# Optimization experiments

Measured on AMD Instinct MI355X. Metric: run time of the kernel, lower is better.

The kernel has to match this reference:

```python
import jax, jax.numpy as jnp
import numpy as np

S, D, H = 2048, 2048, 16
HD = D // H  # head dim = 128
LN_EPS = 1e-5


def _ln(x, g, b):
    mu = jnp.mean(x, axis=-1, keepdims=True)
    var = jnp.var(x, axis=-1, keepdims=True)
    return (x - mu) / jnp.sqrt(var + LN_EPS) * g + b


def setup_inputs() -> dict:
    key = jax.random.key(0)
    ks = jax.random.split(key, 8)
    B = 2
    s = 0.02  # weight init scale
    return {
        "x": jax.random.normal(ks[0], (B, S, D), jnp.float32),
        "Wq": jax.random.normal(ks[1], (D, D), jnp.float32) * s,
        "bq": jnp.zeros((D,), jnp.float32),
        "Wk": jax.random.normal(ks[2], (D, D), jnp.float32) * s,
        "bk": jnp.zeros((D,), jnp.float32),
        "Wv": jax.random.normal(ks[3], (D, D), jnp.float32) * s,
        "bv": jnp.zeros((D,), jnp.float32),
        "Wo": jax.random.normal(ks[4], (D, D), jnp.float32) * s,
        "bo": jnp.zeros((D,), jnp.float32),
        "ln1_g": jnp.ones((D,), jnp.float32),
        "ln1_b": jnp.zeros((D,), jnp.float32),
        "ln2_g": jnp.ones((D,), jnp.float32),
        "ln2_b": jnp.zeros((D,), jnp.float32),
        "W1": jax.random.normal(ks[5], (4 * D, D), jnp.float32) * s,
        "b1": jnp.zeros((4 * D,), jnp.float32),
        "W2": jax.random.normal(ks[6], (D, 4 * D), jnp.float32) * s,
        "b2": jnp.zeros((D,), jnp.float32),
    }


def reference(x, Wq, bq, Wk, bk, Wv, bv, Wo, bo,
              ln1_g, ln1_b, ln2_g, ln2_b, W1, b1, W2, b2):
    causal = jnp.tril(jnp.ones((S, S), bool))  # [S, S] lower-triangular mask
    neg = jnp.finfo(x.dtype).min
    inv_sqrt_hd = 1.0 / jnp.sqrt(jnp.asarray(HD, x.dtype))

    def block(xs):  # xs: [S, D] (equinox module is per-sequence; vmapped over batch)
        h = _ln(xs, ln1_g, ln1_b)
        q = (h @ Wq.T + bq).reshape(S, H, HD)
        k = (h @ Wk.T + bk).reshape(S, H, HD)
        v = (h @ Wv.T + bv).reshape(S, H, HD)
        logits = jnp.einsum('shd,Shd->hsS', q, k) * inv_sqrt_hd
        logits = jnp.where(causal, logits, neg)
        attn = jax.nn.softmax(logits, axis=-1)
        o = jnp.einsum('hsS,Shd->shd', attn, v).reshape(S, D)
        h = h + (o @ Wo.T + bo)          # residual of post-ln1 value (as in source)
        h2 = _ln(h, ln2_g, ln2_b)
        m = jax.nn.gelu(h2 @ W1.T + b1) @ W2.T + b2
        return h2 + m                    # residual of post-ln2 value (as in source)

    return jax.vmap(block)(x)
```

## Files before the change

### kernel.cpp

```cpp
#include <hip/hip_runtime.h>
#include <hip/hip_bf16.h>
#include <math.h>

#define DD   2048
#define SS   2048
#define HH   16
#define HDIM 128
#define BB   2
#define MM   4096
#define D4   8192

using bf16x8 = __attribute__((ext_vector_type(8))) short;
using f32x4  = __attribute__((ext_vector_type(4))) float;
using f32x16 = __attribute__((ext_vector_type(16))) float;

__device__ __forceinline__ ushort f2bf(float x) {
  uint u = __builtin_bit_cast(uint, x);
  u += 0x7FFFu + ((u >> 16) & 1u);
  return (ushort)(u >> 16);
}
__device__ __forceinline__ float bf2f(ushort u) {
  return __builtin_bit_cast(float, (uint)u << 16);
}
__device__ __forceinline__ uint pkbf2(float a, float b) {
  return (uint)f2bf(a) | ((uint)f2bf(b) << 16);
}

__device__ __forceinline__ float gelu_f(float v) {
  float u = 0.7978845608028654f * (v + 0.044715f * v * v * v);
  float e = __expf(2.0f * u);
  float th = 1.0f - 2.0f / (e + 1.0f);
  return 0.5f * v * (1.0f + th);
}

__device__ __forceinline__ void gload_lds16(const void* g, void* l) {
  __builtin_amdgcn_global_load_lds(
      (const __attribute__((address_space(1))) void*)g,
      (__attribute__((address_space(3))) void*)l, 16, 0, 0);
}

template <int SHIFT>
__global__ __launch_bounds__(256) void cvt4_f32_bf16(
    const float* __restrict__ s0, const float* __restrict__ s1,
    const float* __restrict__ s2, const float* __restrict__ s3,
    ushort* __restrict__ dst) {
  int seg = blockIdx.x >> SHIFT;
  int i = ((blockIdx.x & ((1 << SHIFT) - 1)) << 8) + threadIdx.x;
  const float* src = (seg == 0) ? s0 : (seg == 1) ? s1 : (seg == 2) ? s2 : s3;
  float4 v = ((const float4*)src)[i];
  ushort4 o;
  o.x = f2bf(v.x); o.y = f2bf(v.y); o.z = f2bf(v.z); o.w = f2bf(v.w);
  ((ushort4*)dst)[((size_t)seg << (SHIFT + 8)) + i] = o;
}

template <bool BIN>
__global__ __launch_bounds__(256) void ln_rows(
    const void* __restrict__ inp, const float* __restrict__ gam,
    const float* __restrict__ bet, ushort* __restrict__ outb) {
  int row = blockIdx.x;
  int t = threadIdx.x;
  float v[8];
  if (BIN) {
    const ushort4* r4 = (const ushort4*)((const ushort*)inp + (size_t)row * DD);
    ushort4 a = r4[t * 2], b = r4[t * 2 + 1];
    v[0] = bf2f(a.x); v[1] = bf2f(a.y); v[2] = bf2f(a.z); v[3] = bf2f(a.w);
    v[4] = bf2f(b.x); v[5] = bf2f(b.y); v[6] = bf2f(b.z); v[7] = bf2f(b.w);
  } else {
    const float4* r4 = (const float4*)((const float*)inp + (size_t)row * DD);
    float4 a = r4[t * 2], b = r4[t * 2 + 1];
    v[0] = a.x; v[1] = a.y; v[2] = a.z; v[3] = a.w;
    v[4] = b.x; v[5] = b.y; v[6] = b.z; v[7] = b.w;
  }
  float s = ((v[0] + v[1]) + (v[2] + v[3])) + ((v[4] + v[5]) + (v[6] + v[7]));
  __shared__ float redA[4], redB[4];
  #pragma unroll
  for (int off = 32; off >= 1; off >>= 1) s += __shfl_xor(s, off);
  if ((t & 63) == 0) redA[t >> 6] = s;
  __syncthreads();
  float mean = (redA[0] + redA[1] + redA[2] + redA[3]) * (1.0f / DD);
  float q = 0.f;
  #pragma unroll
  for (int i = 0; i < 8; i++) { v[i] -= mean; q += v[i] * v[i]; }
  #pragma unroll
  for (int off = 32; off >= 1; off >>= 1) q += __shfl_xor(q, off);
  if ((t & 63) == 0) redB[t >> 6] = q;
  __syncthreads();
  float var = (redB[0] + redB[1] + redB[2] + redB[3]) * (1.0f / DD);
  float rstd = rsqrtf(var + 1e-5f);
  const float4* g4 = (const float4*)gam;
  const float4* b4 = (const float4*)bet;
  float4 g0 = g4[t * 2], g1 = g4[t * 2 + 1];
  float4 bb0 = b4[t * 2], bb1 = b4[t * 2 + 1];
  ushort4 u0, u1;
  u0.x = f2bf(v[0] * rstd * g0.x + bb0.x);
  u0.y = f2bf(v[1] * rstd * g0.y + bb0.y);
  u0.z = f2bf(v[2] * rstd * g0.z + bb0.z);
  u0.w = f2bf(v[3] * rstd * g0.w + bb0.w);
  u1.x = f2bf(v[4] * rstd * g1.x + bb1.x);
  u1.y = f2bf(v[5] * rstd * g1.y + bb1.y);
  u1.z = f2bf(v[6] * rstd * g1.z + bb1.z);
  u1.w = f2bf(v[7] * rstd * g1.w + bb1.w);
  ushort4* ob4 = (ushort4*)(outb + (size_t)row * DD);
  ob4[t * 2] = u0; ob4[t * 2 + 1] = u1;
}

template <int OMODE, bool GELU_, bool RES_>
__global__ __launch_bounds__(512, 2) void gemm2(
    const ushort* __restrict__ A, const ushort* __restrict__ Bt,
    const float* __restrict__ pb0, const float* __restrict__ pb1,
    const float* __restrict__ pb2, const ushort* __restrict__ res,
    void* __restrict__ Cout, int M, int N, int K) {
  extern __shared__ __align__(16) ushort smem[];
  const int nbm = M >> 8, nbn = N >> 7;
  const int nwg = nbm * nbn;
  int wg = blockIdx.x;
  int wg2 = (wg & 7) * (nwg >> 3) + (wg >> 3);
  int bm = wg2 % nbm, bn = wg2 / nbm;
  int m0 = bm << 8, n0 = bn << 7;
  int t = threadIdx.x, lane = t & 63, w = t >> 6;
  int wm = w >> 2, wn = w & 3;
  int lr = lane & 15, lg = lane >> 4;

  auto stage = [&](int kt, int slot) {
    int k0 = kt << 6;
    ushort* lA = smem + slot * 24576;
    ushort* lB = lA + 16384;
    #pragma unroll
    for (int r = 0; r < 4; r++) {
      int idx = (r << 9) + t;
      int row = idx >> 3, ch = idx & 7;
      gload_lds16(A + (size_t)(m0 + row) * K + k0 + ((ch ^ (row & 7)) << 3),
                  lA + idx * 8);
    }
    #pragma unroll
    for (int r = 0; r < 2; r++) {
      int idx = (r << 9) + t;
      int row = idx >> 3, ch = idx & 7;
      gload_lds16(Bt + (size_t)(n0 + row) * K + k0 + ((ch ^ (row & 7)) << 3),
                  lB + idx * 8);
    }
  };

  f32x4 acc[8][2] = {};
  const int NT = K >> 6;
  stage(0, 0);
  stage(1, 1);
  int slot = 0;
  for (int kt = 0; kt < NT; ++kt) {
    __builtin_amdgcn_sched_barrier(0);
    if (kt + 1 < NT)
      asm volatile("s_waitcnt vmcnt(6)" ::: "memory");
    else
      asm volatile("s_waitcnt vmcnt(0)" ::: "memory");
    __builtin_amdgcn_s_barrier();
    __builtin_amdgcn_sched_barrier(0);
    if (kt + 2 < NT) {
      int s2 = slot + 2; if (s2 >= 3) s2 -= 3;
      stage(kt + 2, s2);
    }
    const ushort* lA = smem + slot * 24576;
    const ushort* lB = lA + 16384;
    bf16x8 af[8][2], bfr[2][2];
    #pragma unroll
    for (int mi = 0; mi < 8; mi++) {
      int row = wm * 128 + mi * 16 + lr;
      #pragma unroll
      for (int ks = 0; ks < 2; ks++)
        af[mi][ks] = *(const bf16x8*)
            &lA[row * 64 + (((ks * 4 + lg) ^ (row & 7)) << 3)];
    }
    #pragma unroll
    for (int ni = 0; ni < 2; ni++) {
      int row = wn * 32 + ni * 16 + lr;
      #pragma unroll
      for (int ks = 0; ks < 2; ks++)
        bfr[ni][ks] = *(const bf16x8*)
            &lB[row * 64 + (((ks * 4 + lg) ^ (row & 7)) << 3)];
    }
    __builtin_amdgcn_s_setprio(1);
    #pragma unroll
    for (int ks = 0; ks < 2; ks++)
      #pragma unroll
      for (int mi = 0; mi < 8; mi++)
        #pragma unroll
        for (int ni = 0; ni < 2; ni++)
          acc[mi][ni] = __builtin_amdgcn_mfma_f32_16x16x32_bf16(
              af[mi][ks], bfr[ni][ks], acc[mi][ni], 0, 0, 0);
    __builtin_amdgcn_s_setprio(0);
    slot = (slot + 1 == 3) ? 0 : slot + 1;
  }

  if (OMODE == 3) {
    int seg = n0 >> 11;
    const float* pb = (seg == 0) ? pb0 : (seg == 1) ? pb1 : pb2;
    int c0 = n0 & 2047;
    float bv[2];
    #pragma unroll
    for (int ni = 0; ni < 2; ni++) bv[ni] = pb[c0 + wn * 32 + ni * 16 + lr];
    if (seg < 2) {
      ushort* q_or_k = (ushort*)Cout + (size_t)seg * MM * DD;
      #pragma unroll
      for (int mi = 0; mi < 8; mi++) {
        #pragma unroll
        for (int r = 0; r < 4; r++) {
          int m = m0 + wm * 128 + mi * 16 + lg * 4 + r;
          #pragma unroll
          for (int ni = 0; ni < 2; ni++) {
            int col = c0 + wn * 32 + ni * 16 + lr;
            q_or_k[(size_t)m * DD + col] = f2bf(acc[mi][ni][r] + bv[ni]);
          }
        }
      }
    } else {
      ushort* vT = (ushort*)Cout + (size_t)2 * MM * DD;
      #pragma unroll
      for (int mi = 0; mi < 8; mi++) {
        int mg = m0 + wm * 128 + mi * 16 + lg * 4;
        int bb_ = mg >> 11, sb = mg & 2047;
        #pragma unroll
        for (int ni = 0; ni < 2; ni++) {
          int col = c0 + wn * 32 + ni * 16 + lr;
          int h = col >> 7, d = col & 127;
          ushort4 u4;
          u4.x = f2bf(acc[mi][ni][0] + bv[ni]);
          u4.y = f2bf(acc[mi][ni][1] + bv[ni]);
          u4.z = f2bf(acc[mi][ni][2] + bv[ni]);
          u4.w = f2bf(acc[mi][ni][3] + bv[ni]);
          size_t idx = ((size_t)(bb_ * 16 + h) * 128 + d) * 2048 + sb;
          *(ushort4*)&vT[idx] = u4;
        }
      }
    }
    return;
  }

  float bv[2];
  #pragma unroll
  for (int ni = 0; ni < 2; ni++) bv[ni] = pb0[n0 + wn * 32 + ni * 16 + lr];
  #pragma unroll
  for (int mi = 0; mi < 8; mi++) {
    #pragma unroll
    for (int r = 0; r < 4; r++) {
      int m = m0 + wm * 128 + mi * 16 + lg * 4 + r;
      #pragma unroll
      for (int ni = 0; ni < 2; ni++) {
        int n = n0 + wn * 32 + ni * 16 + lr;
        size_t idx = (size_t)m * N + n;
        float v = acc[mi][ni][r] + bv[ni];
        if (RES_) v += bf2f(res[idx]);
        if (GELU_) v = gelu_f(v);
        if (OMODE == 1) ((ushort*)Cout)[idx] = f2bf(v);
        else            ((float*)Cout)[idx] = v;
      }
    }
  }
}

#define MF16(MQ, NQ, BARR) \
  { _Pragma("unroll") for (int ks = 0; ks < 2; ks++) { \
    _Pragma("unroll") for (int fm = 0; fm < 4; fm++) { \
      _Pragma("unroll") for (int fn = 0; fn < 2; fn++) { \
        acc[MQ * 4 + fm][NQ * 2 + fn] = \
            __builtin_amdgcn_mfma_f32_16x16x32_bf16( \
                aR[fm][ks], BARR[fn][ks], acc[MQ * 4 + fm][NQ * 2 + fn], \
                0, 0, 0); } } } }

template <int OMODE, bool GELU_>
__global__ __launch_bounds__(512, 2) void gemm8(
    const ushort* __restrict__ A, const ushort* __restrict__ Bt,
    const float* __restrict__ pb0,
    void* __restrict__ Cout, int M, int N, int Kfull) {
  extern __shared__ __align__(16) ushort smem[];
  const int nbm = M >> 8, nbn = N >> 8;
  const int nwg = nbm * nbn;
  int wgr = blockIdx.x;
  int wg2 = (wgr & 7) * (nwg >> 3) + (wgr >> 3);
  int bm = wg2 % nbm, bn = wg2 / nbm;
  int m0 = bm << 8, n0 = bn << 8;
  int t = threadIdx.x, lane = t & 63, w = t >> 6;
  int wm = w >> 2, wn = w & 3;
  int lr = lane & 15, lg = lane >> 4;

  int srow = t >> 3;
  int ssw = ((t & 7) ^ (srow & 7)) << 3;
  const ushort* pA1 = A + (size_t)(m0 + srow) * Kfull + ssw;
  const ushort* pB1 = Bt +
      (size_t)(n0 + (srow >> 5) * 64 + (srow & 31)) * Kfull + ssw;
  const size_t K32 = (size_t)32 * Kfull, K64 = (size_t)64 * Kfull,
               K128 = (size_t)128 * Kfull;
  ushort* dA = smem + t * 8;
  ushort* dB = smem + 16384 + t * 8;

  auto stage = [&](int kt, int h) {
    int boff = (kt & 1) << 15;
    size_t ko = (size_t)kt << 6;
    if (h < 2) {
      const ushort* g = pA1 + (size_t)h * K64 + ko;
      ushort* d = dA + boff + h * 8192;
      gload_lds16(g, d);
      gload_lds16(g + K128, d + 4096);
    } else {
      const ushort* g = pB1 + (size_t)(h - 2) * K32 + ko;
      ushort* d = dB + boff + (h - 2) * 8192;
      gload_lds16(g, d);
      gload_lds16(g + K128, d + 4096);
    }
  };

  int swz0 = (lg ^ (lr & 7)) << 3;
  int swz1 = ((4 + lg) ^ (lr & 7)) << 3;
  int arb[4], brb[2];
  #pragma unroll
  for (int f = 0; f < 4; f++) arb[f] = (wm * 64 + f * 16 + lr) * 64;
  #pragma unroll
  for (int f = 0; f < 2; f++) brb[f] = (wn * 32 + f * 16 + lr) * 64;

  f32x4 acc[8][4] = {};
  bf16x8 aR[4][2], bR0[2][2], bR1[2][2];
  const int NT = Kfull >> 6;

  stage(0, 0); stage(0, 1); stage(0, 2); stage(0, 3);
  stage(1, 0); stage(1, 1); stage(1, 2); stage(1, 3);
  asm volatile("s_waitcnt vmcnt(8)" ::: "memory");
  __builtin_amdgcn_s_barrier();
  __builtin_amdgcn_sched_barrier(0);

  for (int kt = 0; kt < NT; ++kt) {
    const ushort* hA = smem + ((kt & 1) << 15);
    const ushort* hB = hA + 16384;
    bool st2 = (kt + 2 < NT);
    __builtin_amdgcn_s_setprio(1);
    #pragma unroll
    for (int f = 0; f < 4; f++) {
      aR[f][0] = *(const bf16x8*)&hA[arb[f] + swz0];
      aR[f][1] = *(const bf16x8*)&hA[arb[f] + swz1];
    }
    #pragma unroll
    for (int f = 0; f < 2; f++) {
      bR0[f][0] = *(const bf16x8*)&hB[brb[f] + swz0];
      bR0[f][1] = *(const bf16x8*)&hB[brb[f] + swz1];
    }
    MF16(0, 0, bR0);
    __builtin_amdgcn_s_setprio(0);
    __builtin_amdgcn_sched_barrier(0);
    __builtin_amdgcn_s_barrier();
    __builtin_amdgcn_sched_barrier(0);
    if (st2) { stage(kt + 2, 0); stage(kt + 2, 2); }
    __builtin_amdgcn_s_setprio(1);
    #pragma unroll
    for (int f = 0; f < 2; f++) {
      bR1[f][0] = *(const bf16x8*)&hB[8192 + brb[f] + swz0];
      bR1[f][1] = *(const bf16x8*)&hB[8192 + brb[f] + swz1];
    }
    MF16(0, 1, bR1);
    __builtin_amdgcn_s_setprio(0);
    __builtin_amdgcn_sched_barrier(0);
    __builtin_amdgcn_s_barrier();
    __builtin_amdgcn_sched_barrier(0);
    if (st2) stage(kt + 2, 3);
    __builtin_amdgcn_s_setprio(1);
    #pragma unroll
    for (int f = 0; f < 4; f++) {
      aR[f][0] = *(const bf16x8*)&hA[8192 + arb[f] + swz0];
      aR[f][1] = *(const bf16x8*)&hA[8192 + arb[f] + swz1];
    }
    MF16(1, 1, bR1);
    __builtin_amdgcn_s_setprio(0);
    __builtin_amdgcn_sched_barrier(0);
    __builtin_amdgcn_s_barrier();
    __builtin_amdgcn_sched_barrier(0);
    if (st2) stage(kt + 2, 1);
    __builtin_amdgcn_s_setprio(1);
    MF16(1, 0, bR0);
    __builtin_amdgcn_s_setprio(0);
    __builtin_amdgcn_sched_barrier(0);
    if (st2)              { asm volatile("s_waitcnt vmcnt(8)" ::: "memory"); }
    else if (kt + 1 < NT) { asm volatile("s_waitcnt vmcnt(0)" ::: "memory"); }
    __builtin_amdgcn_s_barrier();
    __builtin_amdgcn_sched_barrier(0);
  }

  float bv[4];
  #pragma unroll
  for (int ni = 0; ni < 4; ni++) bv[ni] = pb0[n0 + wn * 64 + ni * 16 + lr];
  #pragma unroll
  for (int mi = 0; mi < 8; mi++) {
    #pragma unroll
    for (int r = 0; r < 4; r++) {
      int m = m0 + wm * 128 + mi * 16 + lg * 4 + r;
      #pragma unroll
      for (int ni = 0; ni < 4; ni++) {
        int n = n0 + wn * 64 + ni * 16 + lr;
        float v = acc[mi][ni][r] + bv[ni];
        if (GELU_) v = gelu_f(v);
        ((ushort*)Cout)[(size_t)m * N + n] = f2bf(v);
      }
    }
  }
}

__global__ __launch_bounds__(256) void attn_fwd(
    const ushort* __restrict__ qb, const ushort* __restrict__ kb,
    const ushort* __restrict__ vTb, ushort* __restrict__ ob) {
  extern __shared__ __align__(16) ushort asm_[];
  ushort* KsB = asm_;
  ushort* VsB = asm_ + 16384;
  ushort* Pw  = asm_ + 32768 + (threadIdx.x >> 6) * 2048;

  int blk = blockIdx.x;
  int i15 = blk & 15;
  int qt = (blk & 256) ? i15 : 15 - i15;
  int bh = blk >> 4;
  int b = bh >> 4, h = bh & 15;
  int q0 = qt << 7;
  int t = threadIdx.x, lane = t & 63, w = t >> 6;
  int l31 = lane & 31, hi = lane >> 5;
  const size_t base = (size_t)b * SS * DD + (size_t)h * HDIM;
  const ushort* qp = qb + base;
  const ushort* kp = kb + base;
  const ushort* vp = vTb + (size_t)bh * HDIM * SS;
  int wq0 = q0 + w * 32;
  int qg = wq0 + l31;

  bf16x8 qf[8];
  #pragma unroll
  for (int kk = 0; kk < 8; kk++)
    qf[kk] = *(const bf16x8*)(qp + (size_t)qg * DD + kk * 16 + hi * 8);

  auto stageKV = [&](int it, int buf) {
    int kv0 = it * 64;
    ushort* Kd = KsB + buf * 8192;
    ushort* Vd = VsB + buf * 8192;
    #pragma unroll
    for (int ii = 0; ii < 4; ii++) {
      int chunk = ii * 256 + t;
      int row = chunk >> 4, cc = chunk & 15;
      gload_lds16(kp + (size_t)(kv0 + row) * DD + ((cc ^ (row & 15)) << 3),
                  Kd + chunk * 8);
    }
    #pragma unroll
    for (int ii = 0; ii < 4; ii++) {
      int chunk = ii * 256 + t;
      int row = chunk >> 3, cc = chunk & 7;
      gload_lds16(vp + (size_t)row * SS + kv0 + ((cc ^ (row & 7)) << 3),
                  Vd + chunk * 8);
    }
  };

  f32x16 o[4] = {};
  float mu = -1e30f, lrow = 0.f;
  const float csc = 0.08838834764831845f * 1.4426950408889634f;

  int nIter = 2 * qt + 2;
  stageKV(0, 0);
  asm volatile("s_waitcnt vmcnt(0)" ::: "memory");
  __builtin_amdgcn_s_barrier();
  int cur = 0;
  for (int it = 0; it < nIter; ++it) {
    int kv0 = it * 64;
    if (it + 1 < nIter) stageKV(it + 1, cur ^ 1);

    if (kv0 <= wq0 + 31) {
      const ushort* Kc = KsB + cur * 8192;
      const ushort* Vc = VsB + cur * 8192;
      f32x16 s2[2] = {};
      #pragma unroll
      for (int nt = 0; nt < 2; nt++) {
        int row = nt * 32 + l31;
        #pragma unroll
        for (int kk = 0; kk < 8; kk++) {
          bf16x8 kf = *(const bf16x8*)
              &Kc[row * 128 + (((kk * 2 + hi) ^ (row & 15)) << 3)];
          s2[nt] = __builtin_amdgcn_mfma_f32_32x32x16_bf16(kf, qf[kk], s2[nt],
                                                           0, 0, 0);
        }
      }
      bool full = (kv0 + 63 <= wq0);
      float pm[4] = {-3e38f, -3e38f, -3e38f, -3e38f};
      if (full) {
        #pragma unroll
        for (int nt = 0; nt < 2; nt++)
          #pragma unroll
          for (int g2 = 0; g2 < 4; g2++)
            #pragma unroll
            for (int i = 0; i < 4; i++) {
              float u = s2[nt][g2 * 4 + i] * csc;
              s2[nt][g2 * 4 + i] = u;
              pm[i] = fmaxf(pm[i], u);
            }
      } else {
        #pragma unroll
        for (int nt = 0; nt < 2; nt++)
          #pragma unroll
          for (int g2 = 0; g2 < 4; g2++)
            #pragma unroll
            for (int i = 0; i < 4; i++) {
              int kvl = nt * 32 + g2 * 8 + 4 * hi + i;
              float u = (kv0 + kvl > qg) ? -3e38f : s2[nt][g2 * 4 + i] * csc;
              s2[nt][g2 * 4 + i] = u;
              pm[i] = fmaxf(pm[i], u);
            }
      }
      float mx = fmaxf(fmaxf(pm[0], pm[1]), fmaxf(pm[2], pm[3]));
      mx = fmaxf(mx, __shfl_xor(mx, 32));
      if (!__all(mx - mu <= 8.0f)) {
        float mnew = fmaxf(mu, mx);
        float fr = exp2f(mu - mnew);
        mu = mnew;
        lrow *= fr;
        #pragma unroll
        for (int dt = 0; dt < 4; dt++)
          #pragma unroll
          for (int r = 0; r < 16; r++) o[dt][r] *= fr;
      }
      float ps[4] = {0.f, 0.f, 0.f, 0.f};
      #pragma unroll
      for (int nt = 0; nt < 2; nt++)
        #pragma unroll
        for (int g2 = 0; g2 < 4; g2++)
          #pragma unroll
          for (int i = 0; i < 4; i++) {
            float p = exp2f(s2[nt][g2 * 4 + i] - mu);
            s2[nt][g2 * 4 + i] = p;
            ps[i] += p;
          }
      float sum = (ps[0] + ps[1]) + (ps[2] + ps[3]);
      sum += __shfl_xor(sum, 32);
      lrow += sum;
      #pragma unroll
      for (int nt = 0; nt < 2; nt++) {
        #pragma unroll
        for (int g2 = 0; g2 < 4; g2++) {
          uint2 u;
          u.x = pkbf2(s2[nt][g2 * 4 + 0], s2[nt][g2 * 4 + 1]);
          u.y = pkbf2(s2[nt][g2 * 4 + 2], s2[nt][g2 * 4 + 3]);
          int cp = (nt * 4 + g2) ^ (l31 & 7);
          *(uint2*)&Pw[l31 * 64 + cp * 8 + hi * 4] = u;
        }
      }
      asm volatile("s_waitcnt lgkmcnt(0)" ::: "memory");
      #pragma unroll
      for (int kk = 0; kk < 4; kk++) {
        bf16x8 pf = *(const bf16x8*)
            &Pw[l31 * 64 + (((kk * 2 + hi) ^ (l31 & 7)) << 3)];
        #pragma unroll
        for (int dt = 0; dt < 4; dt++) {
          int drow = dt * 32 + l31;
          bf16x8 vf = *(const bf16x8*)
              &Vc[drow * 64 + (((kk * 2 + hi) ^ (drow & 7)) << 3)];
          o[dt] = __builtin_amdgcn_mfma_f32_32x32x16_bf16(vf, pf, o[dt],
                                                          0, 0, 0);
        }
      }
    }
    asm volatile("s_waitcnt vmcnt(0)" ::: "memory");
    __builtin_amdgcn_s_barrier();
    cur ^= 1;
  }

  float inv = 1.0f / lrow;
  #pragma unroll
  for (int dt = 0; dt < 4; dt++) {
    #pragma unroll
    for (int g2 = 0; g2 < 4; g2++) {
      uint2 u;
      u.x = pkbf2(o[dt][g2 * 4 + 0] * inv, o[dt][g2 * 4 + 1] * inv);
      u.y = pkbf2(o[dt][g2 * 4 + 2] * inv, o[dt][g2 * 4 + 3] * inv);
      int d = dt * 32 + 8 * g2 + 4 * hi;
      *(uint2*)&ob[base + (size_t)qg * DD + d] = u;
    }
  }
}

extern "C" void kernel_launch(void* const* d_in, const int* in_sizes, int n_in,
                              void* d_out, int out_size, void* d_ws,
                              size_t ws_size, hipStream_t stream) {
  const float* x    = (const float*)d_in[0];
  const float* Wq   = (const float*)d_in[1];
  const float* bq   = (const float*)d_in[2];
  const float* Wk   = (const float*)d_in[3];
  const float* bk   = (const float*)d_in[4];
  const float* Wv   = (const float*)d_in[5];
  const float* bv   = (const float*)d_in[6];
  const float* Wo   = (const float*)d_in[7];
  const float* bo   = (const float*)d_in[8];
  const float* ln1g = (const float*)d_in[9];
  const float* ln1b = (const float*)d_in[10];
  const float* ln2g = (const float*)d_in[11];
  const float* ln2b = (const float*)d_in[12];
  const float* W1   = (const float*)d_in[13];
  const float* b1   = (const float*)d_in[14];
  const float* W2   = (const float*)d_in[15];
  const float* b2   = (const float*)d_in[16];

  char* ws = (char*)d_ws;
  ushort* Wqkvb = (ushort*)(ws);
  ushort* Wob   = Wqkvb + (size_t)3 * DD * DD;
  ushort* W1b = (ushort*)(ws);
  ushort* W2b = W1b + (size_t)D4 * DD;
  ushort* qkvb = (ushort*)(ws + 67108864);
  ushort* qbf = qkvb;
  ushort* kbf = qbf + (size_t)MM * DD;
  ushort* vTt = kbf + (size_t)MM * DD;
  ushort* aob = vTt + (size_t)MM * DD;
  ushort* gb  = (ushort*)(ws + 67108864);
  ushort* hb  = (ushort*)(ws + 167772160);
  ushort* h2b = hb;
  ushort* h2inB = (ushort*)(ws + 184549376);
  float* out  = (float*)d_out;

  const int LDSB = 147456;
  const int LDSC = 131072;
  const int LDSA = 81920;
  (void)hipFuncSetAttribute((const void*)gemm2<3, false, false>,
                      hipFuncAttributeMaxDynamicSharedMemorySize, LDSB);
  (void)hipFuncSetAttribute((const void*)gemm2<1, false, true>,
                      hipFuncAttributeMaxDynamicSharedMemorySize, LDSB);
  (void)hipFuncSetAttribute((const void*)gemm2<0, false, true>,
                      hipFuncAttributeMaxDynamicSharedMemorySize, LDSB);
  (void)hipFuncSetAttribute((const void*)gemm8<1, true>,
                      hipFuncAttributeMaxDynamicSharedMemorySize, LDSC);
  (void)hipFuncSetAttribute((const void*)attn_fwd,
                      hipFuncAttributeMaxDynamicSharedMemorySize, LDSA);

  dim3 blk(256);
  dim3 gblk(512);
  cvt4_f32_bf16<12><<<16384, blk, 0, stream>>>(Wq, Wk, Wv, Wo, Wqkvb);
  ln_rows<false><<<MM, blk, 0, stream>>>(x, ln1g, ln1b, hb);
  gemm2<3, false, false><<<768, gblk, LDSB, stream>>>(
      hb, Wqkvb, bq, bk, bv, nullptr, qkvb, MM, 3 * DD, DD);
  attn_fwd<<<512, blk, LDSA, stream>>>(qbf, kbf, vTt, aob);
  gemm2<1, false, true><<<256, gblk, LDSB, stream>>>(
      aob, Wob, bo, bo, bo, hb, h2inB, MM, DD, DD);
  ln_rows<true><<<MM, blk, 0, stream>>>(h2inB, ln2g, ln2b, h2b);
  cvt4_f32_bf16<14><<<32768, blk, 0, stream>>>(W1, W2, W2, W2, W1b);
  gemm8<1, true><<<512, gblk, LDSC, stream>>>(
      h2b, W1b, b1, gb, MM, D4, DD);
  gemm2<0, false, true><<<256, gblk, LDSB, stream>>>(
      gb, W2b, b2, b2, b2, h2b, out, MM, DD, D4);
}
```

Before: 597.4 us.

## Split-K the MLP down-projection with gemm8 and add a reduction kernel

```diff
diff --git a/kernel.cpp b/kernel.cpp
--- a/kernel.cpp
+++ b/kernel.cpp
@@ -269,42 +269,42 @@
 __global__ __launch_bounds__(512, 2) void gemm8(
     const ushort* __restrict__ A, const ushort* __restrict__ Bt,
     const float* __restrict__ pb0,
-    void* __restrict__ Cout, int M, int N, int Kfull) {
+    void* __restrict__ Cout, int M, int N, int Kfull, int Kloc) {
   extern __shared__ __align__(16) ushort smem[];
   const int nbm = M >> 8, nbn = N >> 8;
   const int nwg = nbm * nbn;
   int wgr = blockIdx.x;
+  int ksl = 0;
+  if (OMODE == 4) { ksl = wgr / nwg; wgr -= ksl * nwg; }
   int wg2 = (wgr & 7) * (nwg >> 3) + (wgr >> 3);
   int bm = wg2 % nbm, bn = wg2 / nbm;
   int m0 = bm << 8, n0 = bn << 8;
+  size_t kbase = (size_t)ksl * Kloc;
   int t = threadIdx.x, lane = t & 63, w = t >> 6;
   int wm = w >> 2, wn = w & 3;
   int lr = lane & 15, lg = lane >> 4;
 
   int srow = t >> 3;
   int ssw = ((t & 7) ^ (srow & 7)) << 3;
-  const ushort* pA1 = A + (size_t)(m0 + srow) * Kfull + ssw;
+  const ushort* pA1 = A + (size_t)(m0 + srow) * Kfull + kbase + ssw;
   const ushort* pB1 = Bt +
-      (size_t)(n0 + (srow >> 5) * 64 + (srow & 31)) * Kfull + ssw;
+      (size_t)(n0 + (srow >> 5) * 64 + (srow & 31)) * Kfull + kbase + ssw;
   const size_t K32 = (size_t)32 * Kfull, K64 = (size_t)64 * Kfull,
                K128 = (size_t)128 * Kfull;
   ushort* dA = smem + t * 8;
   ushort* dB = smem + 16384 + t * 8;
 
-  auto stage = [&](int kt, int h) {
+  auto stage4 = [&](int kt) {
     int boff = (kt & 1) << 15;
     size_t ko = (size_t)kt << 6;
-    if (h < 2) {
-      const ushort* g = pA1 + (size_t)h * K64 + ko;
-      ushort* d = dA + boff + h * 8192;
-      gload_lds16(g, d);
-      gload_lds16(g + K128, d + 4096);
-    } else {
-      const ushort* g = pB1 + (size_t)(h - 2) * K32 + ko;
-      ushort* d = dB + boff + (h - 2) * 8192;
-      gload_lds16(g, d);
-      gload_lds16(g + K128, d + 4096);
-    }
+    gload_lds16(pA1 + ko, dA + boff);
+    gload_lds16(pA1 + K128 + ko, dA + boff + 4096);
+    gload_lds16(pA1 + K64 + ko, dA + boff + 8192);
+    gload_lds16(pA1 + K64 + K128 + ko, dA + boff + 12288);
+    gload_lds16(pB1 + ko, dB + boff);
+    gload_lds16(pB1 + K128 + ko, dB + boff + 4096);
+    gload_lds16(pB1 + K32 + ko, dB + boff + 8192);
+    gload_lds16(pB1 + K32 + K128 + ko, dB + boff + 12288);
   };
 
   int swz0 = (lg ^ (lr & 7)) << 3;
@@ -317,10 +317,9 @@
 
   f32x4 acc[8][4] = {};
   bf16x8 aR[4][2], bR0[2][2], bR1[2][2];
-  const int NT = Kfull >> 6;
-
-  stage(0, 0); stage(0, 1); stage(0, 2); stage(0, 3);
-  stage(1, 0); stage(1, 1); stage(1, 2); stage(1, 3);
+  const int NT = Kloc >> 6;
+
+  stage4(0); stage4(1);
   asm volatile("s_waitcnt vmcnt(8)" ::: "memory");
   __builtin_amdgcn_s_barrier();
   __builtin_amdgcn_sched_barrier(0);
@@ -339,25 +338,13 @@
     for (int f = 0; f < 2; f++) {
       bR0[f][0] = *(const bf16x8*)&hB[brb[f] + swz0];
       bR0[f][1] = *(const bf16x8*)&hB[brb[f] + swz1];
-    }
-    MF16(0, 0, bR0);
-    __builtin_amdgcn_s_setprio(0);
-    __builtin_amdgcn_sched_barrier(0);
-    __builtin_amdgcn_s_barrier();
-    __builtin_amdgcn_sched_barrier(0);
-    if (st2) { stage(kt + 2, 0); stage(kt + 2, 2); }
-    __builtin_amdgcn_s_setprio(1);
-    #pragma unroll
-    for (int f = 0; f < 2; f++) {
       bR1[f][0] = *(const bf16x8*)&hB[8192 + brb[f] + swz0];
       bR1[f][1] = *(const bf16x8*)&hB[8192 + brb[f] + swz1];
     }
+    MF16(0, 0, bR0);
     MF16(0, 1, bR1);
     __builtin_amdgcn_s_setprio(0);
     __builtin_amdgcn_sched_barrier(0);
-    __builtin_amdgcn_s_barrier();
-    __builtin_amdgcn_sched_barrier(0);
-    if (st2) stage(kt + 2, 3);
     __builtin_amdgcn_s_setprio(1);
     #pragma unroll
     for (int f = 0; f < 4; f++) {
@@ -369,7 +356,7 @@
     __builtin_amdgcn_sched_barrier(0);
     __builtin_amdgcn_s_barrier();
     __builtin_amdgcn_sched_barrier(0);
-    if (st2) stage(kt + 2, 1);
+    if (st2) stage4(kt + 2);
     __builtin_amdgcn_s_setprio(1);
     MF16(1, 0, bR0);
     __builtin_amdgcn_s_setprio(0);
@@ -380,23 +367,55 @@
     __builtin_amdgcn_sched_barrier(0);
   }
 
-  float bv[4];
-  #pragma unroll
-  for (int ni = 0; ni < 4; ni++) bv[ni] = pb0[n0 + wn * 64 + ni * 16 + lr];
-  #pragma unroll
-  for (int mi = 0; mi < 8; mi++) {
-    #pragma unroll
-    for (int r = 0; r < 4; r++) {
-      int m = m0 + wm * 128 + mi * 16 + lg * 4 + r;
-      #pragma unroll
-      for (int ni = 0; ni < 4; ni++) {
-        int n = n0 + wn * 64 + ni * 16 + lr;
-        float v = acc[mi][ni][r] + bv[ni];
-        if (GELU_) v = gelu_f(v);
-        ((ushort*)Cout)[(size_t)m * N + n] = f2bf(v);
-      }
-    }
-  }
+  if constexpr (OMODE == 4) {
+    ushort* Cp = (ushort*)Cout + (size_t)ksl * M * N;
+    #pragma unroll
+    for (int mi = 0; mi < 8; mi++) {
+      #pragma unroll
+      for (int r = 0; r < 4; r++) {
+        int m = m0 + wm * 128 + mi * 16 + lg * 4 + r;
+        #pragma unroll
+        for (int ni = 0; ni < 4; ni++) {
+          int n = n0 + wn * 64 + ni * 16 + lr;
+          Cp[(size_t)m * N + n] = f2bf(acc[mi][ni][r]);
+        }
+      }
+    }
+  } else {
+    float bv[4];
+    #pragma unroll
+    for (int ni = 0; ni < 4; ni++) bv[ni] = pb0[n0 + wn * 64 + ni * 16 + lr];
+    #pragma unroll
+    for (int mi = 0; mi < 8; mi++) {
+      #pragma unroll
+      for (int r = 0; r < 4; r++) {
+        int m = m0 + wm * 128 + mi * 16 + lg * 4 + r;
+        #pragma unroll
+        for (int ni = 0; ni < 4; ni++) {
+          int n = n0 + wn * 64 + ni * 16 + lr;
+          float v = acc[mi][ni][r] + bv[ni];
+          if (GELU_) v = gelu_f(v);
+          ((ushort*)Cout)[(size_t)m * N + n] = f2bf(v);
+        }
+      }
+    }
+  }
+}
+
+__global__ __launch_bounds__(256) void mlp_fin(
+    const ushort* __restrict__ p, const ushort* __restrict__ res,
+    const float* __restrict__ bias, float* __restrict__ out) {
+  int i4 = blockIdx.x * 256 + threadIdx.x;
+  ushort4 a = ((const ushort4*)p)[i4];
+  ushort4 b = ((const ushort4*)(p + (size_t)MM * DD))[i4];
+  ushort4 r = ((const ushort4*)res)[i4];
+  float4 g = ((const float4*)bias)[i4 & 511];
+  float4 o;
+  o.x = bf2f(a.x) + bf2f(b.x) + bf2f(r.x) + g.x;
+  o.y = bf2f(a.y) + bf2f(b.y) + bf2f(r.y) + g.y;
+  o.z = bf2f(a.z) + bf2f(b.z) + bf2f(r.z) + g.z;
+  o.w = bf2f(a.w) + bf2f(b.w) + bf2f(r.w) + g.w;
+  ((float4*)out)[i4] = o;
 }
 
 __global__ __launch_bounds__(256) void attn_fwd(
@@ -607,6 +626,7 @@
   ushort* hb  = (ushort*)(ws + 167772160);
   ushort* h2b = hb;
   ushort* h2inB = (ushort*)(ws + 184549376);
+  ushort* pD    = (ushort*)(ws + 184549376);
   float* out  = (float*)d_out;
 
   const int LDSB = 147456;
@@ -616,9 +636,9 @@
                       hipFuncAttributeMaxDynamicSharedMemorySize, LDSB);
   (void)hipFuncSetAttribute((const void*)gemm2<1, false, true>,
                       hipFuncAttributeMaxDynamicSharedMemorySize, LDSB);
-  (void)hipFuncSetAttribute((const void*)gemm2<0, false, true>,
-                      hipFuncAttributeMaxDynamicSharedMemorySize, LDSB);
   (void)hipFuncSetAttribute((const void*)gemm8<1, true>,
+                      hipFuncAttributeMaxDynamicSharedMemorySize, LDSC);
+  (void)hipFuncSetAttribute((const void*)gemm8<4, false>,
                       hipFuncAttributeMaxDynamicSharedMemorySize, LDSC);
   (void)hipFuncSetAttribute((const void*)attn_fwd,
                       hipFuncAttributeMaxDynamicSharedMemorySize, LDSA);
@@ -635,7 +655,8 @@
   ln_rows<true><<<MM, blk, 0, stream>>>(h2inB, ln2g, ln2b, h2b);
   cvt4_f32_bf16<14><<<32768, blk, 0, stream>>>(W1, W2, W2, W2, W1b);
   gemm8<1, true><<<512, gblk, LDSC, stream>>>(
-      h2b, W1b, b1, gb, MM, D4, DD);
-  gemm2<0, false, true><<<256, gblk, LDSB, stream>>>(
-      gb, W2b, b2, b2, b2, h2b, out, MM, DD, D4);
-}
+      h2b, W1b, b1, gb, MM, D4, DD, DD);
+  gemm8<4, false><<<256, gblk, LDSC, stream>>>(
+      gb, W2b, b2, pD, MM, DD, D4, D4 / 2);
+  mlp_fin<<<MM * DD / 1024, blk, 0, stream>>>(pD, h2b, b2, out);
+}
```

Result: no change. 605.3 us (+1.3%).
